# Optimization experiments

Hardware: AMD Instinct MI355X
Metric: run time of the kernel (lower is better)

## Reference

```python
import jax, jax.numpy as jnp
import numpy as np


def _conv(x, k):
    # x: (B,H,W,Cin), k: (kh,kw,Cin,Cout), SAME padding, stride 1
    return jax.lax.conv_general_dilated(
        x, k, window_strides=(1, 1), padding='SAME',
        dimension_numbers=('NHWC', 'HWIO', 'NHWC'))


def _hard_sigmoid(x):
    # Keras ConvLSTM2D default recurrent_activation='hard_sigmoid'
    return jnp.clip(0.2 * x + 0.5, 0.0, 1.0)


def _convlstm_layer(x_seq, k, rk, b):
    # x_seq: (B,T,H,W,Cin); gates packed i,f,c,o along channel axis (Keras order)
    B, T, H, W, _ = x_seq.shape
    F = rk.shape[2]
    h0 = jnp.zeros((B, H, W, F), x_seq.dtype)
    c0 = jnp.zeros((B, H, W, F), x_seq.dtype)

    def step(carry, xt):
        h, c = carry
        z = _conv(xt, k) + _conv(h, rk) + b
        i, f, g, o = jnp.split(z, 4, axis=-1)
        c_new = _hard_sigmoid(f) * c + _hard_sigmoid(i) * jnp.tanh(g)
        h_new = _hard_sigmoid(o) * jnp.tanh(c_new)
        return (h_new, c_new), h_new

    (h, c), ys = jax.lax.scan(step, (h0, c0), jnp.moveaxis(x_seq, 1, 0))
    return jnp.moveaxis(ys, 0, 1), h, c  # outputs (B,T,H,W,F), final h, c


def setup_inputs() -> dict:
    key = jax.random.key(0)
    ks = jax.random.split(key, 6)
    s = 0.05
    return {
        'x': jax.random.normal(ks[0], (8, 10, 64, 64, 1), jnp.float32),
        'k0': jax.random.normal(ks[1], (3, 3, 1, 256), jnp.float32) * s,
        'rk0': jax.random.normal(ks[2], (3, 3, 64, 256), jnp.float32) * s,
        'b0': jnp.zeros((256,), jnp.float32),
        'k1': jax.random.normal(ks[3], (3, 3, 64, 256), jnp.float32) * s,
        'rk1': jax.random.normal(ks[4], (3, 3, 64, 256), jnp.float32) * s,
        'b1': jnp.zeros((256,), jnp.float32),
    }


def reference(x, k0, rk0, b0, k1, rk1, b1):
    # layer 0
    seq0, h0, c0 = _convlstm_layer(x, k0, rk0, b0)
    # layer 1 consumes layer-0 sequence
    _, h1, c1 = _convlstm_layer(seq0, k1, rk1, b1)
    # states list [[h0,c0],[h1,c1]] -> stacked (layers=2, 2, B, H, W, F)
    return jnp.stack([jnp.stack([h0, c0]), jnp.stack([h1, c1])])
```

## Files before the change

kernel.cpp:

```cpp
#include <hip/hip_runtime.h>
#include <hip/hip_bf16.h>

typedef unsigned short u16;
typedef __attribute__((ext_vector_type(8))) short short8;
typedef __attribute__((ext_vector_type(4))) float f32x4;

#define T_STEPS 10
#define NB 8
#define HH 64
#define WW 64
#define FF 64
#define NGATE 256
#define HP 66
#define PIX (NB*HH*WW)

__device__ __forceinline__ u16 f2bf(float f) {
    unsigned u = __float_as_uint(f);
    u += 0x7FFF + ((u >> 16) & 1);
    return (u16)(u >> 16);
}
__device__ __forceinline__ float hsig(float x) {
    return fminf(fmaxf(0.2f * x + 0.5f, 0.0f), 1.0f);
}
__device__ __forceinline__ float ftanh(float x) {
    float e = __expf(2.0f * x);
    return 1.0f - 2.0f / (e + 1.0f);
}
__device__ __forceinline__ void gll16(const void* g, void* l) {
    __builtin_amdgcn_global_load_lds(
        (const __attribute__((address_space(1))) unsigned*)g,
        (__attribute__((address_space(3))) unsigned*)l, 16, 0, 0);
}

__global__ void wtrans_kernel(const float* __restrict__ W0,
                              const float* __restrict__ W1,
                              u16* __restrict__ BS, int K) {
    int total = (K >> 6) << 14;
    for (int o = blockIdx.x * blockDim.x + threadIdx.x; o < total;
         o += gridDim.x * blockDim.x) {
        int e = o & 7, lane = (o >> 3) & 63, g = (o >> 9) & 3;
        int ks = (o >> 11) & 1, fq = (o >> 12) & 3, kc = o >> 14;
        int quad = lane >> 4, l15 = lane & 15;
        int n = g * 64 + fq * 16 + l15;
        int k = kc * 64 + ks * 32 + quad * 8 + e;
        float v = (k < 576) ? W0[k * NGATE + n] : W1[(k - 576) * NGATE + n];
        BS[o] = f2bf(v);
    }
}

__global__ __launch_bounds__(256, 4)
void fused_step_kernel(const u16* __restrict__ h0_prev, u16* __restrict__ h0_new,
                       const u16* __restrict__ h1_prev, u16* __restrict__ h1_new,
                       const u16* __restrict__ B0S, const u16* __restrict__ B1S,
                       const float* __restrict__ x, const float* __restrict__ k0w,
                       const float* __restrict__ b0, const float* __restrict__ b1,
                       float* __restrict__ c0, float* __restrict__ c1,
                       float* __restrict__ oh0, float* __restrict__ oc0,
                       float* __restrict__ oh1, float* __restrict__ oc1,
                       int u) {
    int blk = blockIdx.x;
    int role = blk & 1;
    int pxb = blk >> 1;
    if (role == 0 && u >= T_STEPS) return;
    if (role == 1 && u == 0) return;

    __shared__ __align__(16) u16 sA2[2][4096];
    __shared__ float xs[3][WW + 2];

    int tid = threadIdx.x;
    int lane = tid & 63, fq = tid >> 6;
    int quad = lane >> 4, l15 = lane & 15;
    int b = pxb >> 6, y = pxb & 63;

    const u16* BS = role ? B1S : B0S;
    int nch = role ? 18 : 9;

    if (role == 0 && tid < 3 * (WW + 2)) {
        int dyi = tid / (WW + 2), xx = tid - dyi * (WW + 2);
        int yy = y + dyi - 1, col = xx - 1;
        float v = 0.0f;
        if (yy >= 0 && yy < HH && col >= 0 && col < WW)
            v = x[(((size_t)b * T_STEPS + u) * HH + yy) * WW + col];
        xs[dyi][xx] = v;
    }

    int q0 = tid, q1 = 256 + tid;
    int p0 = q0 >> 3, s0 = q0 & 7, cb0 = s0 ^ (p0 & 7);
    int p1 = q1 >> 3, s1 = q1 & 7, cb1 = s1 ^ (p1 & 7);

#define STAGE(KC, BUF)                                                        \
    {                                                                         \
        int tau_ = ((KC) < 9) ? (KC) : (KC) - 9;                              \
        const u16* src_ = ((KC) < 9) ? h0_prev : h1_prev;                     \
        int dy_ = tau_ / 3 - 1, dx_ = tau_ % 3 - 1;                           \
        const u16* rbase_ = src_ + (((size_t)(b * HP + y + dy_ + 1)) * HP +   \
                                    dx_ + 1) * FF;                            \
        gll16(rbase_ + (size_t)p0 * FF + cb0 * 8, &sA2[BUF][(size_t)q0 * 8]); \
        gll16(rbase_ + (size_t)p1 * FF + cb1 * 8, &sA2[BUF][(size_t)q1 * 8]); \
    }

    f32x4 acc[4][4];
#pragma unroll
    for (int mt = 0; mt < 4; ++mt)
#pragma unroll
        for (int g = 0; g < 4; ++g)
            acc[mt][g] = (f32x4){0.f, 0.f, 0.f, 0.f};

    STAGE(0, 0);
    __syncthreads();

    int sx = l15 & 7;
    for (int kc = 0; kc < nch; ++kc) {
        int cur = kc & 1;
        const u16* bst = BS + (((size_t)kc << 14) | (fq << 12)) + (size_t)lane * 8;
        short8 bAll[8];
#pragma unroll
        for (int j = 0; j < 8; ++j)
            bAll[j] = *(const short8*)(bst + ((size_t)j << 9));
        if (kc + 1 < nch) STAGE(kc + 1, cur ^ 1);
#pragma unroll
        for (int ks = 0; ks < 2; ++ks) {
            short8 aF[4];
#pragma unroll
            for (int mt = 0; mt < 4; ++mt) {
                int px = mt * 16 + l15;
                int chunk = px * 8 + ((ks * 4 + quad) ^ sx);
                aF[mt] = *(const short8*)&sA2[cur][(size_t)chunk * 8];
            }
#pragma unroll
            for (int mt = 0; mt < 4; ++mt)
#pragma unroll
                for (int g = 0; g < 4; ++g)
                    acc[mt][g] = __builtin_amdgcn_mfma_f32_16x16x32_bf16(
                        aF[mt], bAll[ks * 4 + g], acc[mt][g], 0, 0, 0);
        }
        __syncthreads();
    }

    const float* bias = role ? b1 : b0;
    float* cbuf = role ? c1 : c0;
    u16* hout = role ? h1_new : h0_new;
    int wo = role ? (u == T_STEPS) : (u == T_STEPS - 1);
    float* outh = role ? oh1 : oh0;
    float* outc = role ? oc1 : oc0;

    int f = fq * 16 + l15;
    float bi = bias[f], bff = bias[64 + f], bg = bias[128 + f], bo = bias[192 + f];
    float wk[4][9];
    if (role == 0) {
#pragma unroll
        for (int g = 0; g < 4; ++g)
#pragma unroll
            for (int tau = 0; tau < 9; ++tau)
                wk[g][tau] = k0w[tau * NGATE + g * 64 + f];
    }
#pragma unroll
    for (int mt = 0; mt < 4; ++mt) {
#pragma unroll
        for (int r = 0; r < 4; ++r) {
            int xcol = mt * 16 + quad * 4 + r;
            size_t p = (size_t)pxb * 64 + xcol;
            float zi = acc[mt][0][r] + bi;
            float zf = acc[mt][1][r] + bff;
            float zg = acc[mt][2][r] + bg;
            float zo = acc[mt][3][r] + bo;
            if (role == 0) {
#pragma unroll
                for (int tau = 0; tau < 9; ++tau) {
                    float xv = xs[tau / 3][xcol + tau % 3];
                    zi += xv * wk[0][tau];
                    zf += xv * wk[1][tau];
                    zg += xv * wk[2][tau];
                    zo += xv * wk[3][tau];
                }
            }
            float cold = cbuf[p * FF + f];
            float cn = hsig(zf) * cold + hsig(zi) * ftanh(zg);
            float hn = hsig(zo) * ftanh(cn);
            cbuf[p * FF + f] = cn;
            hout[(((size_t)(b * HP + y + 1)) * HP + (xcol + 1)) * FF + f] = f2bf(hn);
            if (wo) { outh[p * FF + f] = hn; outc[p * FF + f] = cn; }
        }
    }
}

extern "C" void kernel_launch(void* const* d_in, const int* in_sizes, int n_in,
                              void* d_out, int out_size, void* d_ws, size_t ws_size,
                              hipStream_t stream) {
    const float* x   = (const float*)d_in[0];
    const float* k0  = (const float*)d_in[1];
    const float* rk0 = (const float*)d_in[2];
    const float* b0  = (const float*)d_in[3];
    const float* k1  = (const float*)d_in[4];
    const float* rk1 = (const float*)d_in[5];
    const float* b1  = (const float*)d_in[6];
    float* out = (float*)d_out;

    char* ws = (char*)d_ws;
    const size_t HPAD_BYTES = (size_t)NB * HP * HP * FF * 2;
    const size_t C_BYTES    = (size_t)PIX * FF * 4;

    u16* h0p[2]; u16* h1p[2];
    h0p[0] = (u16*)(ws);
    h0p[1] = (u16*)(ws + HPAD_BYTES);
    h1p[0] = (u16*)(ws + 2 * HPAD_BYTES);
    h1p[1] = (u16*)(ws + 3 * HPAD_BYTES);
    float* c0 = (float*)(ws + 4 * HPAD_BYTES);
    float* c1 = (float*)(ws + 4 * HPAD_BYTES + C_BYTES);
    u16* B0S  = (u16*)(ws + 4 * HPAD_BYTES + 2 * C_BYTES);
    u16* B1S  = (u16*)(ws + 4 * HPAD_BYTES + 2 * C_BYTES + (size_t)9 * 16384 * 2);

    hipMemsetAsync(ws, 0, 4 * HPAD_BYTES + 2 * C_BYTES, stream);

    wtrans_kernel<<<512, 256, 0, stream>>>(rk0, rk0, B0S, 576);
    wtrans_kernel<<<512, 256, 0, stream>>>(k1, rk1, B1S, 1152);

    float* oh0 = out;
    float* oc0 = out + (size_t)PIX * FF;
    float* oh1 = out + 2 * (size_t)PIX * FF;
    float* oc1 = out + 3 * (size_t)PIX * FF;

    for (int u = 0; u <= T_STEPS; ++u) {
        const u16* h0_prev = h0p[(u + 1) & 1];
        u16*       h0_new  = h0p[u & 1];
        const u16* h1_prev = h1p[u & 1];
        u16*       h1_new  = h1p[(u + 1) & 1];
        fused_step_kernel<<<1024, 256, 0, stream>>>(
            h0_prev, h0_new, h1_prev, h1_new, B0S, B1S,
            x, k0, b0, b1, c0, c1, oh0, oc0, oh1, oc1, u);
    }
}
```

Baseline: 534.5 us.

## Triple-buffer LDS A tiles with vmcnt-gated barriers and remap block order

```diff
diff --git a/kernel.cpp b/kernel.cpp
--- a/kernel.cpp
+++ b/kernel.cpp
@@ -48,6 +48,19 @@
     }
 }
 
+__device__ __forceinline__ void stageA(const u16* __restrict__ h0_prev,
+                                       const u16* __restrict__ h1_prev,
+                                       int kcs, int b, int y,
+                                       int p0, int cb0, int p1, int cb1,
+                                       u16* ldst0, u16* ldst1) {
+    int tau = (kcs < 9) ? kcs : kcs - 9;
+    const u16* src = (kcs < 9) ? h0_prev : h1_prev;
+    int dy = tau / 3 - 1, dx = tau % 3 - 1;
+    const u16* rbase = src + (((size_t)(b * HP + y + dy + 1)) * HP + dx + 1) * FF;
+    gll16(rbase + (size_t)p0 * FF + cb0 * 8, ldst0);
+    gll16(rbase + (size_t)p1 * FF + cb1 * 8, ldst1);
+}
+
 __global__ __launch_bounds__(256, 4)
 void fused_step_kernel(const u16* __restrict__ h0_prev, u16* __restrict__ h0_new,
                        const u16* __restrict__ h1_prev, u16* __restrict__ h1_new,
@@ -59,18 +72,19 @@
                        float* __restrict__ oh1, float* __restrict__ oc1,
                        int u) {
     int blk = blockIdx.x;
-    int role = blk & 1;
-    int pxb = blk >> 1;
+    int b = blk & 7;
+    int role = (blk >> 3) & 1;
+    int y = blk >> 4;
+    int pxb = b * 64 + y;
     if (role == 0 && u >= T_STEPS) return;
     if (role == 1 && u == 0) return;
 
-    __shared__ __align__(16) u16 sA2[2][4096];
+    __shared__ __align__(16) u16 sA3[3][4096];
     __shared__ float xs[3][WW + 2];
 
     int tid = threadIdx.x;
     int lane = tid & 63, fq = tid >> 6;
     int quad = lane >> 4, l15 = lane & 15;
-    int b = pxb >> 6, y = pxb & 63;
 
     const u16* BS = role ? B1S : B0S;
     int nch = role ? 18 : 9;
@@ -85,19 +99,8 @@
     }
 
     int q0 = tid, q1 = 256 + tid;
-    int p0 = q0 >> 3, s0 = q0 & 7, cb0 = s0 ^ (p0 & 7);
-    int p1 = q1 >> 3, s1 = q1 & 7, cb1 = s1 ^ (p1 & 7);
-
-#define STAGE(KC, BUF)                                                        \
-    {                                                                         \
-        int tau_ = ((KC) < 9) ? (KC) : (KC) - 9;                              \
-        const u16* src_ = ((KC) < 9) ? h0_prev : h1_prev;                     \
-        int dy_ = tau_ / 3 - 1, dx_ = tau_ % 3 - 1;                           \
-        const u16* rbase_ = src_ + (((size_t)(b * HP + y + dy_ + 1)) * HP +   \
-                                    dx_ + 1) * FF;                            \
-        gll16(rbase_ + (size_t)p0 * FF + cb0 * 8, &sA2[BUF][(size_t)q0 * 8]); \
-        gll16(rbase_ + (size_t)p1 * FF + cb1 * 8, &sA2[BUF][(size_t)q1 * 8]); \
-    }
+    int p0 = q0 >> 3, cb0 = (q0 & 7) ^ (p0 & 7);
+    int p1 = q1 >> 3, cb1 = (q1 & 7) ^ (p1 & 7);
 
     f32x4 acc[4][4];
 #pragma unroll
@@ -106,35 +109,46 @@
         for (int g = 0; g < 4; ++g)
             acc[mt][g] = (f32x4){0.f, 0.f, 0.f, 0.f};
 
-    STAGE(0, 0);
-    __syncthreads();
+    stageA(h0_prev, h1_prev, 0, b, y, p0, cb0, p1, cb1,
+           &sA3[0][(size_t)q0 * 8], &sA3[0][(size_t)q1 * 8]);
+    asm volatile("s_waitcnt vmcnt(0) lgkmcnt(0)\n\ts_barrier" ::: "memory");
+    if (nch > 1)
+        stageA(h0_prev, h1_prev, 1, b, y, p0, cb0, p1, cb1,
+               &sA3[1][(size_t)q0 * 8], &sA3[1][(size_t)q1 * 8]);
 
     int sx = l15 & 7;
+    int cur = 0;
     for (int kc = 0; kc < nch; ++kc) {
-        int cur = kc & 1;
-        const u16* bst = BS + (((size_t)kc << 14) | (fq << 12)) + (size_t)lane * 8;
-        short8 bAll[8];
-#pragma unroll
-        for (int j = 0; j < 8; ++j)
-            bAll[j] = *(const short8*)(bst + ((size_t)j << 9));
-        if (kc + 1 < nch) STAGE(kc + 1, cur ^ 1);
 #pragma unroll
         for (int ks = 0; ks < 2; ++ks) {
+            short8 bF[4];
+            const u16* bp = BS + (((size_t)kc << 14) | (fq << 12) | (ks << 11))
+                          + lane * 8;
+#pragma unroll
+            for (int g = 0; g < 4; ++g)
+                bF[g] = *(const short8*)(bp + ((size_t)g << 9));
             short8 aF[4];
 #pragma unroll
             for (int mt = 0; mt < 4; ++mt) {
                 int px = mt * 16 + l15;
                 int chunk = px * 8 + ((ks * 4 + quad) ^ sx);
-                aF[mt] = *(const short8*)&sA2[cur][(size_t)chunk * 8];
+                aF[mt] = *(const short8*)&sA3[cur][(size_t)chunk * 8];
             }
 #pragma unroll
             for (int mt = 0; mt < 4; ++mt)
 #pragma unroll
                 for (int g = 0; g < 4; ++g)
                     acc[mt][g] = __builtin_amdgcn_mfma_f32_16x16x32_bf16(
-                        aF[mt], bAll[ks * 4 + g], acc[mt][g], 0, 0, 0);
+                        aF[mt], bF[g], acc[mt][g], 0, 0, 0);
         }
-        __syncthreads();
+        {
+            int ksrc = (kc + 2 < nch) ? kc + 2 : kc;
+            int bdst = (cur + 2 >= 3) ? cur - 1 : cur + 2;
+            stageA(h0_prev, h1_prev, ksrc, b, y, p0, cb0, p1, cb1,
+                   &sA3[bdst][(size_t)q0 * 8], &sA3[bdst][(size_t)q1 * 8]);
+        }
+        asm volatile("s_waitcnt vmcnt(2) lgkmcnt(0)\n\ts_barrier" ::: "memory");
+        cur = (cur == 2) ? 0 : cur + 1;
     }
 
     const float* bias = role ? b1 : b0;
```

After: 507.7 us. 5.0% less time.

## Stage full padded input rows in LDS once and reuse across conv taps

Applied to the files above, without the earlier changes.

```diff
diff --git a/kernel.cpp b/kernel.cpp
--- a/kernel.cpp
+++ b/kernel.cpp
@@ -13,6 +13,7 @@
 #define NGATE 256
 #define HP 66
 #define PIX (NB*HH*WW)
+#define ROWCH 528
 
 __device__ __forceinline__ u16 f2bf(float f) {
     unsigned u = __float_as_uint(f);
@@ -48,7 +49,7 @@
     }
 }
 
-__global__ __launch_bounds__(256, 4)
+__global__ __launch_bounds__(256, 3)
 void fused_step_kernel(const u16* __restrict__ h0_prev, u16* __restrict__ h0_new,
                        const u16* __restrict__ h1_prev, u16* __restrict__ h1_new,
                        const u16* __restrict__ B0S, const u16* __restrict__ B1S,
@@ -59,21 +60,25 @@
                        float* __restrict__ oh1, float* __restrict__ oc1,
                        int u) {
     int blk = blockIdx.x;
-    int role = blk & 1;
-    int pxb = blk >> 1;
+    int b = blk & 7;
+    int k = blk >> 3;
+    int c = k & 31, s = k >> 5;
+    int role = (c + s) & 1;
+    int y = c + ((s >> 1) << 5);
+    int pxb = b * 64 + y;
     if (role == 0 && u >= T_STEPS) return;
     if (role == 1 && u == 0) return;
 
-    __shared__ __align__(16) u16 sA2[2][4096];
+    __shared__ __align__(16) u16 sRows[3328 * 8];
     __shared__ float xs[3][WW + 2];
 
     int tid = threadIdx.x;
     int lane = tid & 63, fq = tid >> 6;
     int quad = lane >> 4, l15 = lane & 15;
-    int b = pxb >> 6, y = pxb & 63;
 
     const u16* BS = role ? B1S : B0S;
-    int nch = role ? 18 : 9;
+    int nrows = role ? 6 : 3;
+    int nstage = nrows * ROWCH;
 
     if (role == 0 && tid < 3 * (WW + 2)) {
         int dyi = tid / (WW + 2), xx = tid - dyi * (WW + 2);
@@ -84,20 +89,18 @@
         xs[dyi][xx] = v;
     }
 
-    int q0 = tid, q1 = 256 + tid;
-    int p0 = q0 >> 3, s0 = q0 & 7, cb0 = s0 ^ (p0 & 7);
-    int p1 = q1 >> 3, s1 = q1 & 7, cb1 = s1 ^ (p1 & 7);
-
-#define STAGE(KC, BUF)                                                        \
-    {                                                                         \
-        int tau_ = ((KC) < 9) ? (KC) : (KC) - 9;                              \
-        const u16* src_ = ((KC) < 9) ? h0_prev : h1_prev;                     \
-        int dy_ = tau_ / 3 - 1, dx_ = tau_ % 3 - 1;                           \
-        const u16* rbase_ = src_ + (((size_t)(b * HP + y + dy_ + 1)) * HP +   \
-                                    dx_ + 1) * FF;                            \
-        gll16(rbase_ + (size_t)p0 * FF + cb0 * 8, &sA2[BUF][(size_t)q0 * 8]); \
-        gll16(rbase_ + (size_t)p1 * FF + cb1 * 8, &sA2[BUF][(size_t)q1 * 8]); \
-    }
+    for (int j = 0; j < 13; ++j) {
+        int q = tid + j * 256;
+        if (q < nstage) {
+            int r = q / ROWCH, rem = q - r * ROWCH;
+            int px = rem >> 3, cb = (rem & 7) ^ (px & 7);
+            const u16* src = (r < 3) ? h0_prev : h1_prev;
+            int grow = y + ((r < 3) ? r : r - 3);
+            gll16(src + ((size_t)(b * HP + grow) * HP + px) * FF + cb * 8,
+                  &sRows[(size_t)q * 8]);
+        }
+    }
+    asm volatile("s_waitcnt vmcnt(0) lgkmcnt(0)\n\ts_barrier" ::: "memory");
 
     f32x4 acc[4][4];
 #pragma unroll
@@ -106,35 +109,42 @@
         for (int g = 0; g < 4; ++g)
             acc[mt][g] = (f32x4){0.f, 0.f, 0.f, 0.f};
 
-    STAGE(0, 0);
-    __syncthreads();
-
-    int sx = l15 & 7;
-    for (int kc = 0; kc < nch; ++kc) {
-        int cur = kc & 1;
-        const u16* bst = BS + (((size_t)kc << 14) | (fq << 12)) + (size_t)lane * 8;
-        short8 bAll[8];
-#pragma unroll
-        for (int j = 0; j < 8; ++j)
-            bAll[j] = *(const short8*)(bst + ((size_t)j << 9));
-        if (kc + 1 < nch) STAGE(kc + 1, cur ^ 1);
-#pragma unroll
-        for (int ks = 0; ks < 2; ++ks) {
-            short8 aF[4];
-#pragma unroll
-            for (int mt = 0; mt < 4; ++mt) {
-                int px = mt * 16 + l15;
-                int chunk = px * 8 + ((ks * 4 + quad) ^ sx);
-                aF[mt] = *(const short8*)&sA2[cur][(size_t)chunk * 8];
-            }
-#pragma unroll
-            for (int mt = 0; mt < 4; ++mt)
-#pragma unroll
-                for (int g = 0; g < 4; ++g)
-                    acc[mt][g] = __builtin_amdgcn_mfma_f32_16x16x32_bf16(
-                        aF[mt], bAll[ks * 4 + g], acc[mt][g], 0, 0, 0);
+#define TAP(KC, ROWBASE, DX)                                                  \
+    {                                                                         \
+        const u16* bp = BS + ((size_t)(KC) << 14) + (fq << 12) + lane * 8;    \
+        short8 bF[8];                                                         \
+        _Pragma("unroll")                                                     \
+        for (int j = 0; j < 8; ++j)                                           \
+            bF[j] = *(const short8*)(bp + ((size_t)j << 9));                  \
+        _Pragma("unroll")                                                     \
+        for (int ks = 0; ks < 2; ++ks) {                                      \
+            short8 aF[4];                                                     \
+            _Pragma("unroll")                                                 \
+            for (int mt = 0; mt < 4; ++mt) {                                  \
+                int px = mt * 16 + l15 + (DX) + 1;                            \
+                int chunk = (ROWBASE) + px * 8 + ((ks * 4 + quad) ^ (px & 7));\
+                aF[mt] = *(const short8*)&sRows[(size_t)chunk * 8];           \
+            }                                                                 \
+            _Pragma("unroll")                                                 \
+            for (int mt = 0; mt < 4; ++mt)                                    \
+                _Pragma("unroll")                                             \
+                for (int g = 0; g < 4; ++g)                                   \
+                    acc[mt][g] = __builtin_amdgcn_mfma_f32_16x16x32_bf16(     \
+                        aF[mt], bF[ks * 4 + g], acc[mt][g], 0, 0, 0);         \
+        }                                                                     \
+    }
+
+    if (role == 0) {
+#pragma unroll
+        for (int kc = 0; kc < 9; ++kc)
+            TAP(kc, (kc / 3) * ROWCH, kc % 3 - 1);
+    } else {
+#pragma unroll
+        for (int kc = 0; kc < 18; ++kc) {
+            int t = (kc < 9) ? kc : kc - 9;
+            int row = ((kc < 9) ? 0 : 3) + t / 3;
+            TAP(kc, row * ROWCH, t % 3 - 1);
         }
-        __syncthreads();
     }
 
     const float* bias = role ? b1 : b0;
```

Measured after the change: 517.2 us. 1.03x faster.

## Stage three padded rows once per block and split layer-1 work across two blocks

Applied to the files above, without the earlier changes.

```diff
diff --git a/kernel.cpp b/kernel.cpp
--- a/kernel.cpp
+++ b/kernel.cpp
@@ -13,6 +13,8 @@
 #define NGATE 256
 #define HP 66
 #define PIX (NB*HH*WW)
+#define ROWCH 528
+#define STAGECH (3*ROWCH)
 
 __device__ __forceinline__ u16 f2bf(float f) {
     unsigned u = __float_as_uint(f);
@@ -30,6 +32,12 @@
     __builtin_amdgcn_global_load_lds(
         (const __attribute__((address_space(1))) unsigned*)g,
         (__attribute__((address_space(3))) unsigned*)l, 16, 0, 0);
+}
+__device__ __forceinline__ void lds_barrier() {
+    asm volatile("s_waitcnt lgkmcnt(0)\n\ts_barrier" ::: "memory");
+}
+__device__ __forceinline__ void full_barrier() {
+    asm volatile("s_waitcnt vmcnt(0) lgkmcnt(0)\n\ts_barrier" ::: "memory");
 }
 
 __global__ void wtrans_kernel(const float* __restrict__ W0,
@@ -48,7 +56,7 @@
     }
 }
 
-__global__ __launch_bounds__(256, 4)
+__global__ __launch_bounds__(256, 6)
 void fused_step_kernel(const u16* __restrict__ h0_prev, u16* __restrict__ h0_new,
                        const u16* __restrict__ h1_prev, u16* __restrict__ h1_new,
                        const u16* __restrict__ B0S, const u16* __restrict__ B1S,
@@ -59,21 +67,22 @@
                        float* __restrict__ oh1, float* __restrict__ oc1,
                        int u) {
     int blk = blockIdx.x;
-    int role = blk & 1;
-    int pxb = blk >> 1;
+    int b = blk & 7;
+    int k = blk >> 3;
+    int role = (k >= 64);
+    int idx = role ? (k - 64) : k;
+    int y = role ? (idx >> 1) : idx;
+    int nh = role ? (idx & 1) : 0;
+    int pxb = b * 64 + y;
     if (role == 0 && u >= T_STEPS) return;
     if (role == 1 && u == 0) return;
 
-    __shared__ __align__(16) u16 sA2[2][4096];
+    __shared__ __align__(16) u16 sRows[STAGECH * 8];
     __shared__ float xs[3][WW + 2];
 
     int tid = threadIdx.x;
-    int lane = tid & 63, fq = tid >> 6;
+    int lane = tid & 63, wv = tid >> 6;
     int quad = lane >> 4, l15 = lane & 15;
-    int b = pxb >> 6, y = pxb & 63;
-
-    const u16* BS = role ? B1S : B0S;
-    int nch = role ? 18 : 9;
 
     if (role == 0 && tid < 3 * (WW + 2)) {
         int dyi = tid / (WW + 2), xx = tid - dyi * (WW + 2);
@@ -84,87 +93,73 @@
         xs[dyi][xx] = v;
     }
 
-    int q0 = tid, q1 = 256 + tid;
-    int p0 = q0 >> 3, s0 = q0 & 7, cb0 = s0 ^ (p0 & 7);
-    int p1 = q1 >> 3, s1 = q1 & 7, cb1 = s1 ^ (p1 & 7);
-
-#define STAGE(KC, BUF)                                                        \
-    {                                                                         \
-        int tau_ = ((KC) < 9) ? (KC) : (KC) - 9;                              \
-        const u16* src_ = ((KC) < 9) ? h0_prev : h1_prev;                     \
-        int dy_ = tau_ / 3 - 1, dx_ = tau_ % 3 - 1;                           \
-        const u16* rbase_ = src_ + (((size_t)(b * HP + y + dy_ + 1)) * HP +   \
-                                    dx_ + 1) * FF;                            \
-        gll16(rbase_ + (size_t)p0 * FF + cb0 * 8, &sA2[BUF][(size_t)q0 * 8]); \
-        gll16(rbase_ + (size_t)p1 * FF + cb1 * 8, &sA2[BUF][(size_t)q1 * 8]); \
-    }
-
-    f32x4 acc[4][4];
-#pragma unroll
-    for (int mt = 0; mt < 4; ++mt)
-#pragma unroll
-        for (int g = 0; g < 4; ++g)
-            acc[mt][g] = (f32x4){0.f, 0.f, 0.f, 0.f};
-
-    STAGE(0, 0);
-    __syncthreads();
-
-    int sx = l15 & 7;
-    for (int kc = 0; kc < nch; ++kc) {
-        int cur = kc & 1;
-        const u16* bst = BS + (((size_t)kc << 14) | (fq << 12)) + (size_t)lane * 8;
-        short8 bAll[8];
-#pragma unroll
-        for (int j = 0; j < 8; ++j)
-            bAll[j] = *(const short8*)(bst + ((size_t)j << 9));
-        if (kc + 1 < nch) STAGE(kc + 1, cur ^ 1);
-#pragma unroll
-        for (int ks = 0; ks < 2; ++ks) {
-            short8 aF[4];
-#pragma unroll
-            for (int mt = 0; mt < 4; ++mt) {
-                int px = mt * 16 + l15;
-                int chunk = px * 8 + ((ks * 4 + quad) ^ sx);
-                aF[mt] = *(const short8*)&sA2[cur][(size_t)chunk * 8];
-            }
-#pragma unroll
-            for (int mt = 0; mt < 4; ++mt)
-#pragma unroll
-                for (int g = 0; g < 4; ++g)
-                    acc[mt][g] = __builtin_amdgcn_mfma_f32_16x16x32_bf16(
-                        aF[mt], bAll[ks * 4 + g], acc[mt][g], 0, 0, 0);
-        }
-        __syncthreads();
-    }
-
-    const float* bias = role ? b1 : b0;
-    float* cbuf = role ? c1 : c0;
-    u16* hout = role ? h1_new : h0_new;
-    int wo = role ? (u == T_STEPS) : (u == T_STEPS - 1);
-    float* outh = role ? oh1 : oh0;
-    float* outc = role ? oc1 : oc0;
-
-    int f = fq * 16 + l15;
-    float bi = bias[f], bff = bias[64 + f], bg = bias[128 + f], bo = bias[192 + f];
-    float wk[4][9];
+#define STAGE3(SRC)                                                           \
+    for (int j = 0; j < 7; ++j) {                                             \
+        int q = tid + j * 256;                                                \
+        if (q < STAGECH) {                                                    \
+            int r = q / ROWCH, rem = q - r * ROWCH;                           \
+            int px = rem >> 3, cb = (rem & 7) ^ (px & 7);                     \
+            gll16((SRC) + ((size_t)(b * HP + y + r) * HP + px) * FF + cb * 8, \
+                  &sRows[(size_t)q * 8]);                                     \
+        }                                                                     \
+    }
+
     if (role == 0) {
+        f32x4 acc[4][4];
+#pragma unroll
+        for (int mt = 0; mt < 4; ++mt)
+#pragma unroll
+            for (int g = 0; g < 4; ++g)
+                acc[mt][g] = (f32x4){0.f, 0.f, 0.f, 0.f};
+
+        STAGE3(h0_prev);
+        full_barrier();
+
+#pragma unroll
+        for (int kc = 0; kc < 9; ++kc) {
+            int rowbase = (kc / 3) * ROWCH, dx = kc % 3 - 1;
+            const u16* bp = B0S + ((size_t)kc << 14) + (wv << 12) + lane * 8;
+            short8 bF[8];
+#pragma unroll
+            for (int j = 0; j < 8; ++j)
+                bF[j] = *(const short8*)(bp + ((size_t)j << 9));
+#pragma unroll
+            for (int ks = 0; ks < 2; ++ks) {
+                short8 aF[4];
+#pragma unroll
+                for (int mt = 0; mt < 4; ++mt) {
+                    int px = mt * 16 + l15 + dx + 1;
+                    int chunk = rowbase + px * 8 + ((ks * 4 + quad) ^ (px & 7));
+                    aF[mt] = *(const short8*)&sRows[(size_t)chunk * 8];
+                }
+#pragma unroll
+                for (int mt = 0; mt < 4; ++mt)
+#pragma unroll
+                    for (int g = 0; g < 4; ++g)
+                        acc[mt][g] = __builtin_amdgcn_mfma_f32_16x16x32_bf16(
+                            aF[mt], bF[ks * 4 + g], acc[mt][g], 0, 0, 0);
+            }
+        }
+
+        int f = wv * 16 + l15;
+        float bi = b0[f], bff = b0[64 + f], bg = b0[128 + f], bo = b0[192 + f];
+        float wk[4][9];
 #pragma unroll
         for (int g = 0; g < 4; ++g)
 #pragma unroll
             for (int tau = 0; tau < 9; ++tau)
                 wk[g][tau] = k0w[tau * NGATE + g * 64 + f];
-    }
-#pragma unroll
-    for (int mt = 0; mt < 4; ++mt) {
-#pragma unroll
-        for (int r = 0; r < 4; ++r) {
-            int xcol = mt * 16 + quad * 4 + r;
-            size_t p = (size_t)pxb * 64 + xcol;
-            float zi = acc[mt][0][r] + bi;
-            float zf = acc[mt][1][r] + bff;
-            float zg = acc[mt][2][r] + bg;
-            float zo = acc[mt][3][r] + bo;
-            if (role == 0) {
+        int wo = (u == T_STEPS - 1);
+#pragma unroll
+        for (int mt = 0; mt < 4; ++mt) {
+#pragma unroll
+            for (int r = 0; r < 4; ++r) {
+                int xcol = mt * 16 + quad * 4 + r;
+                size_t p = (size_t)pxb * 64 + xcol;
+                float zi = acc[mt][0][r] + bi;
+                float zf = acc[mt][1][r] + bff;
+                float zg = acc[mt][2][r] + bg;
+                float zo = acc[mt][3][r] + bo;
 #pragma unroll
                 for (int tau = 0; tau < 9; ++tau) {
                     float xv = xs[tau / 3][xcol + tau % 3];
@@ -173,13 +168,79 @@
                     zg += xv * wk[2][tau];
                     zo += xv * wk[3][tau];
                 }
-            }
-            float cold = cbuf[p * FF + f];
-            float cn = hsig(zf) * cold + hsig(zi) * ftanh(zg);
-            float hn = hsig(zo) * ftanh(cn);
-            cbuf[p * FF + f] = cn;
-            hout[(((size_t)(b * HP + y + 1)) * HP + (xcol + 1)) * FF + f] = f2bf(hn);
-            if (wo) { outh[p * FF + f] = hn; outc[p * FF + f] = cn; }
+                float cold = c0[p * FF + f];
+                float cn = hsig(zf) * cold + hsig(zi) * ftanh(zg);
+                float hn = hsig(zo) * ftanh(cn);
+                c0[p * FF + f] = cn;
+                h0_new[(((size_t)(b * HP + y + 1)) * HP + (xcol + 1)) * FF + f] = f2bf(hn);
+                if (wo) { oh0[p * FF + f] = hn; oc0[p * FF + f] = cn; }
+            }
+        }
+    } else {
+        int mh = wv >> 1, fh = wv & 1;
+        int fqs = nh * 2 + fh;
+        f32x4 acc[2][4];
+#pragma unroll
+        for (int mt = 0; mt < 2; ++mt)
+#pragma unroll
+            for (int g = 0; g < 4; ++g)
+                acc[mt][g] = (f32x4){0.f, 0.f, 0.f, 0.f};
+
+        STAGE3(h0_prev);
+        full_barrier();
+
+#pragma unroll
+        for (int kc = 0; kc < 18; ++kc) {
+            if (kc == 9) {
+                lds_barrier();
+                STAGE3(h1_prev);
+                full_barrier();
+            }
+            int t = (kc < 9) ? kc : kc - 9;
+            int rowbase = (t / 3) * ROWCH, dx = t % 3 - 1;
+            const u16* bp = B1S + ((size_t)kc << 14) + (fqs << 12) + lane * 8;
+            short8 bF[8];
+#pragma unroll
+            for (int j = 0; j < 8; ++j)
+                bF[j] = *(const short8*)(bp + ((size_t)j << 9));
+#pragma unroll
+            for (int ks = 0; ks < 2; ++ks) {
+                short8 aF[2];
+#pragma unroll
+                for (int mt = 0; mt < 2; ++mt) {
+                    int px = mh * 32 + mt * 16 + l15 + dx + 1;
+                    int chunk = rowbase + px * 8 + ((ks * 4 + quad) ^ (px & 7));
+                    aF[mt] = *(const short8*)&sRows[(size_t)chunk * 8];
+                }
+#pragma unroll
+                for (int mt = 0; mt < 2; ++mt)
+#pragma unroll
+                    for (int g = 0; g < 4; ++g)
+                        acc[mt][g] = __builtin_amdgcn_mfma_f32_16x16x32_bf16(
+                            aF[mt], bF[ks * 4 + g], acc[mt][g], 0, 0, 0);
+            }
+        }
+
+        int f = nh * 32 + fh * 16 + l15;
+        float bi = b1[f], bff = b1[64 + f], bg = b1[128 + f], bo = b1[192 + f];
+        int wo = (u == T_STEPS);
+#pragma unroll
+        for (int mt = 0; mt < 2; ++mt) {
+#pragma unroll
+            for (int r = 0; r < 4; ++r) {
+                int xcol = mh * 32 + mt * 16 + quad * 4 + r;
+                size_t p = (size_t)pxb * 64 + xcol;
+                float zi = acc[mt][0][r] + bi;
+                float zf = acc[mt][1][r] + bff;
+                float zg = acc[mt][2][r] + bg;
+                float zo = acc[mt][3][r] + bo;
+                float cold = c1[p * FF + f];
+                float cn = hsig(zf) * cold + hsig(zi) * ftanh(zg);
+                float hn = hsig(zo) * ftanh(cn);
+                c1[p * FF + f] = cn;
+                h1_new[(((size_t)(b * HP + y + 1)) * HP + (xcol + 1)) * FF + f] = f2bf(hn);
+                if (wo) { oh1[p * FF + f] = hn; oc1[p * FF + f] = cn; }
+            }
         }
     }
 }
@@ -225,7 +286,7 @@
         u16*       h0_new  = h0p[u & 1];
         const u16* h1_prev = h1p[u & 1];
         u16*       h1_new  = h1p[(u + 1) & 1];
-        fused_step_kernel<<<1024, 256, 0, stream>>>(
+        fused_step_kernel<<<1536, 256, 0, stream>>>(
             h0_prev, h0_new, h1_prev, h1_new, B0S, B1S,
             x, k0, b0, b1, c0, c1, oh0, oc0, oh1, oc1, u);
     }
```

Result: slower. 1.348 ms (+152.2%).
